# Kernel tuning notes

Hardware: AMD Instinct MI355X
Metric: run time of the kernel (lower is better)

## Reference

```python
import jax, jax.numpy as jnp
import numpy as np

DIM = 512
HEADS = 8
HD = DIM // HEADS
HIDDEN = 4 * DIM
EPS = 1e-5


def layernorm(x, g, b):
    mu = jnp.mean(x, axis=-1, keepdims=True)
    var = jnp.mean(jnp.square(x - mu), axis=-1, keepdims=True)
    return (x - mu) * jax.lax.rsqrt(var + EPS) * g + b


def setup_inputs() -> dict:
    key = jax.random.key(0)
    ks = jax.random.split(key, 10)
    B, P, N, C = 16, 4, 256, DIM
    s = 1.0 / np.sqrt(C)
    sh = 1.0 / np.sqrt(HIDDEN)
    return {
        "x": jax.random.normal(ks[0], (B, P, N, C), jnp.float32),
        "ln1_g": jnp.ones((C,), jnp.float32),
        "ln1_b": jnp.zeros((C,), jnp.float32),
        "w_qkv": jax.random.uniform(ks[1], (3 * C, C), jnp.float32, -s, s),
        "w_proj": jax.random.uniform(ks[2], (C, C), jnp.float32, -s, s),
        "b_proj": jax.random.uniform(ks[3], (C,), jnp.float32, -s, s),
        "ln2_g": jnp.ones((C,), jnp.float32),
        "ln2_b": jnp.zeros((C,), jnp.float32),
        "w1": jax.random.uniform(ks[4], (HIDDEN, C), jnp.float32, -s, s),
        "b1": jax.random.uniform(ks[5], (HIDDEN,), jnp.float32, -s, s),
        "w2": jax.random.uniform(ks[6], (C, HIDDEN), jnp.float32, -sh, sh),
        "b2": jax.random.uniform(ks[7], (C,), jnp.float32, -sh, sh),
    }


def reference(x, ln1_g, ln1_b, w_qkv, w_proj, b_proj, ln2_g, ln2_b, w1, b1, w2, b2):
    B, P, N, C = x.shape
    # --- attention branch (batched over B, P, heads; same math as the unrolled loops) ---
    h = layernorm(x, ln1_g, ln1_b)
    qkv = jnp.einsum('bpnc,dc->bpnd', h, w_qkv)            # [B,P,N,3C]
    qkv = qkv.reshape(B, P, N, 3, HEADS, HD)
    q, k, v = qkv[..., 0, :, :], qkv[..., 1, :, :], qkv[..., 2, :, :]  # [B,P,N,H,hd]
    scale = HD ** -0.5
    attn = jnp.einsum('bpnhd,bpmhd->bphnm', q * scale, k)  # [B,P,H,N,N]
    attn = jax.nn.softmax(attn, axis=-1)
    o = jnp.einsum('bphnm,bpmhd->bpnhd', attn, v).reshape(B, P, N, C)
    o = jnp.einsum('bpnc,dc->bpnd', o, w_proj) + b_proj
    x = x + o
    # --- MLP branch ---
    h = layernorm(x, ln2_g, ln2_b)
    h = jax.nn.gelu(jnp.einsum('bpnc,hc->bpnh', h, w1) + b1, approximate=False)
    h = jnp.einsum('bpnh,ch->bpnc', h, w2) + b2
    return x + h
```

## Files before the change

kernel.cpp:

```cpp
#include <hip/hip_runtime.h>

typedef __attribute__((ext_vector_type(8))) short short8;
typedef __attribute__((ext_vector_type(4))) float f32x4;
typedef __attribute__((ext_vector_type(4))) unsigned short u16x4;
typedef __attribute__((ext_vector_type(2))) unsigned int u32x2;
typedef __attribute__((ext_vector_type(4))) unsigned int u32x4;

__device__ __forceinline__ float bf2f(unsigned short u) {
    return __uint_as_float(((unsigned)u) << 16);
}
__device__ __forceinline__ unsigned short f2bf(float f) {
    unsigned u = __float_as_uint(f);
    u += 0x7fffu + ((u >> 16) & 1u);
    return (unsigned short)(u >> 16);
}
__device__ __forceinline__ unsigned pack2(float a, float b) {
    unsigned r;
    asm("v_cvt_pk_bf16_f32 %0, %1, %2" : "=v"(r) : "v"(a), "v"(b));
    return r;
}
__device__ __forceinline__ void load_lds16(const void* g, void* l) {
    __builtin_amdgcn_global_load_lds(
        (const __attribute__((address_space(1))) void*)g,
        (__attribute__((address_space(3))) void*)l, 16, 0, 0);
}
__device__ __forceinline__ bool is_bf16(const unsigned* dt) {
    return *dt == 0x3F803F80u;
}
__device__ __forceinline__ float gelu_fast(float t) {
    float q = t * (1.5957691f + 0.07135482f * t * t);
    float e = __expf(-q);
    return __fdividef(t, 1.0f + e);
}

__global__ __launch_bounds__(512) void cast_all(
    const void* s_wqkv, const void* s_wproj, const void* s_w1, const void* s_w2,
    const void* v0, const void* v1, const void* v2, const void* v3,
    const void* v4, const void* v5, const void* v6,
    unsigned short* d_wqkv, unsigned short* d_wproj, unsigned short* d_w1,
    unsigned short* d_w2, unsigned short* par, const unsigned* dt)
{
    bool isbf = is_bf16(dt);
    int b = blockIdx.x, tid = threadIdx.x;
    if (b < 768) {
        const void* src; unsigned short* dst; int off;
        if (b < 192)      { src = s_wqkv;  dst = d_wqkv;  off = b * 4096; }
        else if (b < 256) { src = s_wproj; dst = d_wproj; off = (b - 192) * 4096; }
        else if (b < 512) { src = s_w1;    dst = d_w1;    off = (b - 256) * 4096; }
        else              { src = s_w2;    dst = d_w2;    off = (b - 512) * 4096; }
        int i = off + tid * 8;
        if (isbf) {
            *(short8*)(dst + i) = *(const short8*)((const unsigned short*)src + i);
        } else {
            const float* s = (const float*)src + i;
            short8 o;
            #pragma unroll
            for (int j = 0; j < 8; ++j) o[j] = (short)f2bf(s[j]);
            *(short8*)(dst + i) = o;
        }
    } else {
        const void* srcs[7]  = {v0, v1, v2, v3, v4, v5, v6};
        const int   sizes[7] = {512, 512, 512, 512, 512, 2048, 512};
        const int   offs[7]  = {0, 512, 1024, 1536, 2048, 2560, 4608};
        int j = b - 768;
        const void* s = srcs[j];
        unsigned short* d = par + offs[j];
        for (int i = tid; i < sizes[j]; i += 512)
            d[i] = isbf ? ((const unsigned short*)s)[i] : f2bf(((const float*)s)[i]);
    }
}

__global__ __launch_bounds__(256) void ln_kernel(
    const void* __restrict__ xin, size_t row0, int isf32,
    const unsigned short* __restrict__ g, const unsigned short* __restrict__ b,
    unsigned short* __restrict__ y)
{
    int w = threadIdx.x >> 6, lane = threadIdx.x & 63;
    size_t lr = (size_t)blockIdx.x * 4 + w;
    size_t gr = row0 + lr;
    float v[8];
    if (isf32) {
        const float* xr = (const float*)xin + (gr << 9) + (lane << 3);
        #pragma unroll
        for (int j = 0; j < 8; ++j) v[j] = xr[j];
    } else {
        short8 raw = *(const short8*)((const unsigned short*)xin + (gr << 9) + (lane << 3));
        #pragma unroll
        for (int j = 0; j < 8; ++j) v[j] = bf2f((unsigned short)raw[j]);
    }
    float sum = 0.f, sq = 0.f;
    #pragma unroll
    for (int j = 0; j < 8; ++j) { sum += v[j]; sq += v[j] * v[j]; }
    #pragma unroll
    for (int off = 32; off > 0; off >>= 1) {
        sum += __shfl_xor(sum, off);
        sq  += __shfl_xor(sq, off);
    }
    float mu  = sum * (1.0f / 512.0f);
    float var = sq * (1.0f / 512.0f) - mu * mu;
    float rs  = rsqrtf(var + 1e-5f);
    short8 gr8 = *(const short8*)(g + (lane << 3));
    short8 br8 = *(const short8*)(b + (lane << 3));
    float o[8];
    #pragma unroll
    for (int j = 0; j < 8; ++j)
        o[j] = (v[j] - mu) * rs * bf2f((unsigned short)gr8[j]) + bf2f((unsigned short)br8[j]);
    u32x4 ov = {pack2(o[0], o[1]), pack2(o[2], o[3]),
                pack2(o[4], o[5]), pack2(o[6], o[7])};
    *(u32x4*)(y + (lr << 9) + (lane << 3)) = ov;
}

__global__ __launch_bounds__(256, 2) void gemm_big(
    const unsigned short* __restrict__ A, const unsigned short* __restrict__ W,
    const unsigned short* __restrict__ bias,
    unsigned short* __restrict__ out,
    int NBY, int N, int K, int mode)
{
    __shared__ char lds[49152];

    int tid = threadIdx.x;
    int w = tid >> 6, lane = tid & 63;
    int l15 = lane & 15, g = lane >> 4;

    int L = blockIdx.x;
    int bx, by;
    if ((NBY & 7) == 0) {
        int nby8 = NBY >> 3;
        int xcd = L & 7, i = L >> 3;
        by = xcd * nby8 + (i % nby8);
        bx = i / nby8;
    } else {
        by = L % NBY;
        bx = L / NBY;
    }
    int m0 = by << 8, n0 = bx << 7;
    int wm = (w >> 1) << 7;
    int wn = (w & 1) << 6;

    int srow = tid >> 3;
    int u = (tid & 7) ^ (srow & 7);
    const unsigned short* gA[8];
    const unsigned short* gB[4];
    #pragma unroll
    for (int j = 0; j < 8; ++j)
        gA[j] = A + (size_t)(m0 + j * 32 + srow) * K + u * 8;
    #pragma unroll
    for (int j = 0; j < 4; ++j)
        gB[j] = W + (size_t)(n0 + j * 32 + srow) * K + u * 8;
    int lslot = tid * 16;
    int swz = l15 & 7;

    f32x4 acc[4][8];
    #pragma unroll
    for (int i = 0; i < 4; ++i)
        #pragma unroll
        for (int j = 0; j < 8; ++j) acc[i][j] = (f32x4){0.f, 0.f, 0.f, 0.f};

    for (int k = 0; k < K; k += 64) {
        if (k > 0) __syncthreads();
        #pragma unroll
        for (int j = 0; j < 8; ++j)
            load_lds16(gA[j] + k, &lds[j * 4096 + lslot]);
        #pragma unroll
        for (int j = 0; j < 4; ++j)
            load_lds16(gB[j] + k, &lds[32768 + j * 4096 + lslot]);
        __syncthreads();
        const char* bAct = lds;
        const char* bW = lds + 32768;
        #pragma unroll
        for (int s = 0; s < 2; ++s) {
            int cs = ((s * 4 + g) ^ swz) << 4;
            short8 wf[4];
            #pragma unroll
            for (int i = 0; i < 4; ++i)
                wf[i] = *(const short8*)(bW + (wn + i * 16 + l15) * 128 + cs);
            #pragma unroll
            for (int jg = 0; jg < 8; jg += 4) {
                short8 af[4];
                #pragma unroll
                for (int j = 0; j < 4; ++j)
                    af[j] = *(const short8*)(bAct + (wm + (jg + j) * 16 + l15) * 128 + cs);
                #pragma unroll
                for (int i = 0; i < 4; ++i)
                    #pragma unroll
                    for (int j = 0; j < 4; ++j)
                        acc[i][jg + j] = __builtin_amdgcn_mfma_f32_16x16x32_bf16(
                            wf[i], af[j], acc[i][jg + j], 0, 0, 0);
            }
        }
    }
    __syncthreads();

    if (mode == 2) {
        #pragma unroll
        for (int i = 0; i < 4; ++i) {
            u16x4 bb = *(const u16x4*)(bias + n0 + wn + i * 16 + g * 4);
            #pragma unroll
            for (int j = 0; j < 8; ++j)
                #pragma unroll
                for (int r = 0; r < 4; ++r)
                    acc[i][j][r] = gelu_fast(acc[i][j][r] + bf2f(bb[r]));
        }
    }

    #pragma unroll
    for (int hh = 0; hh < 2; ++hh) {
        if ((w >> 1) == hh) {
            #pragma unroll
            for (int j = 0; j < 8; ++j) {
                int mloc = j * 16 + l15;
                char* rowp = lds + mloc * 256;
                int sw = mloc & 30;
                #pragma unroll
                for (int i = 0; i < 4; ++i) {
                    int cq = (wn + i * 16 + g * 4) >> 2;
                    u32x2 pk = {pack2(acc[i][j][0], acc[i][j][1]),
                                pack2(acc[i][j][2], acc[i][j][3])};
                    *(u32x2*)(rowp + ((cq ^ sw) << 3)) = pk;
                }
            }
        }
        __syncthreads();
        int rL = tid >> 4, lc = tid & 15;
        int colg = n0 + lc * 8;
        #pragma unroll
        for (int ps = 0; ps < 8; ++ps) {
            int row = ps * 16 + rL;
            int rowL = m0 + hh * 128 + row;
            int c16 = lc ^ ((row >> 1) & 15);
            short8 vv = *(const short8*)(lds + row * 256 + (c16 << 4));
            *(short8*)(out + (size_t)rowL * N + colg) = vv;
        }
        if (hh == 0) __syncthreads();
    }
}

__global__ __launch_bounds__(256) void gemm8(
    const unsigned short* __restrict__ A, const unsigned short* __restrict__ W,
    const unsigned short* __restrict__ bias,
    const void* __restrict__ resid, size_t rrow0,
    void* __restrict__ out, size_t orow0,
    int NBY, int N, int K, int mode, int inbf)
{
    constexpr int BN = 128;
    __shared__ char lds[32768];

    int tid = threadIdx.x;
    int w = tid >> 6, lane = tid & 63;
    int l15 = lane & 15, g = lane >> 4;

    int L = blockIdx.x;
    int bx, by;
    if ((NBY & 7) == 0) {
        int nby8 = NBY >> 3;
        int xcd = L & 7, i = L >> 3;
        by = xcd * nby8 + (i % nby8);
        bx = i / nby8;
    } else {
        by = L % NBY;
        bx = L / NBY;
    }
    int m0 = by << 7, n0 = bx << 7;
    int wm = (w >> 1) << 6;
    int wn = (w & 1) << 6;

    int srow_t = tid >> 3;
    int u_t = (tid & 7) ^ (srow_t & 7);
    const unsigned short* gA[4];
    const unsigned short* gB[4];
    #pragma unroll
    for (int j = 0; j < 4; ++j) {
        gA[j] = A + (size_t)(m0 + j * 32 + srow_t) * K + u_t * 8;
        gB[j] = W + (size_t)(n0 + j * 32 + srow_t) * K + u_t * 8;
    }
    int lslot = tid * 16;
    int swz = l15 & 7;

    f32x4 acc[4][4];
    #pragma unroll
    for (int i = 0; i < 4; ++i)
        #pragma unroll
        for (int j = 0; j < 4; ++j) acc[i][j] = (f32x4){0.f, 0.f, 0.f, 0.f};

    for (int k = 0; k < K; k += 64) {
        if (k > 0) __syncthreads();
        #pragma unroll
        for (int j = 0; j < 4; ++j) {
            load_lds16(gA[j] + k, &lds[j * 4096 + lslot]);
            load_lds16(gB[j] + k, &lds[16384 + j * 4096 + lslot]);
        }
        __syncthreads();
        const char* bAct = lds;
        const char* bW = bAct + 16384;
        #pragma unroll
        for (int s = 0; s < 2; ++s) {
            int cs = ((s * 4 + g) ^ swz) << 4;
            short8 wf[4], af[4];
            #pragma unroll
            for (int i = 0; i < 4; ++i)
                wf[i] = *(const short8*)(bW + (wn + i * 16 + l15) * 128 + cs);
            #pragma unroll
            for (int j = 0; j < 4; ++j)
                af[j] = *(const short8*)(bAct + (wm + j * 16 + l15) * 128 + cs);
            #pragma unroll
            for (int i = 0; i < 4; ++i)
                #pragma unroll
                for (int j = 0; j < 4; ++j)
                    acc[i][j] = __builtin_amdgcn_mfma_f32_16x16x32_bf16(wf[i], af[j], acc[i][j], 0, 0, 0);
        }
    }
    __syncthreads();

    char* tb = (char*)lds;
    #pragma unroll
    for (int j = 0; j < 4; ++j) {
        int mloc = wm + j * 16 + l15;
        char* rowp = tb + mloc * (BN * 2);
        int sw = mloc & (BN / 4 - 2);
        #pragma unroll
        for (int i = 0; i < 4; ++i) {
            int cq = (wn + i * 16 + g * 4) >> 2;
            u32x2 pk = {pack2(acc[i][j][0], acc[i][j][1]),
                        pack2(acc[i][j][2], acc[i][j][3])};
            *(u32x2*)(rowp + ((cq ^ sw) << 3)) = pk;
        }
    }
    __syncthreads();

    int rL = tid >> 4;
    int lc = tid & 15;
    int colg = n0 + lc * 8;
    float bv[8];
    if (mode != 0) {
        short8 bb = *(const short8*)(bias + colg);
        #pragma unroll
        for (int t = 0; t < 8; ++t) bv[t] = bf2f((unsigned short)bb[t]);
    }

    #pragma unroll
    for (int ps = 0; ps < 8; ++ps) {
        int row = ps * 16 + rL;
        int rowL = m0 + row;
        int c16 = lc ^ ((row >> 1) & 15);
        short8 vv = *(const short8*)(tb + row * (BN * 2) + (c16 << 4));

        if (mode == 0) {
            *(short8*)((unsigned short*)out + (size_t)rowL * N + colg) = vv;
        } else if (mode == 1) {
            size_t rbase = (rrow0 + rowL) * (size_t)N + colg;
            float o8[8];
            if (inbf) {
                short8 rr = *(const short8*)((const unsigned short*)resid + rbase);
                #pragma unroll
                for (int t = 0; t < 8; ++t)
                    o8[t] = bf2f((unsigned short)rr[t]) + bf2f((unsigned short)vv[t]) + bv[t];
            } else {
                f32x4 r0 = *(const f32x4*)((const float*)resid + rbase);
                f32x4 r1 = *(const f32x4*)((const float*)resid + rbase + 4);
                #pragma unroll
                for (int t = 0; t < 4; ++t) {
                    o8[t]     = r0[t] + bf2f((unsigned short)vv[t]) + bv[t];
                    o8[t + 4] = r1[t] + bf2f((unsigned short)vv[t + 4]) + bv[t + 4];
                }
            }
            u32x4 ov = {pack2(o8[0], o8[1]), pack2(o8[2], o8[3]),
                        pack2(o8[4], o8[5]), pack2(o8[6], o8[7])};
            *(u32x4*)((unsigned short*)out + (size_t)rowL * N + colg) = ov;
        } else {
            size_t rbase = (size_t)rowL * N + colg;
            short8 rr = *(const short8*)((const unsigned short*)resid + rbase);
            float o8[8];
            #pragma unroll
            for (int t = 0; t < 8; ++t)
                o8[t] = bf2f((unsigned short)rr[t]) + bf2f((unsigned short)vv[t]) + bv[t];
            size_t obase = (orow0 + rowL) * (size_t)N + colg;
            if (inbf) {
                u32x4 ov = {pack2(o8[0], o8[1]), pack2(o8[2], o8[3]),
                            pack2(o8[4], o8[5]), pack2(o8[6], o8[7])};
                *(u32x4*)((unsigned short*)out + obase) = ov;
            } else {
                float* ob = (float*)out + obase;
                *(f32x4*)ob       = (f32x4){o8[0], o8[1], o8[2], o8[3]};
                *(f32x4*)(ob + 4) = (f32x4){o8[4], o8[5], o8[6], o8[7]};
            }
        }
    }
}

__global__ __launch_bounds__(256) void attn_mfma(
    const unsigned short* __restrict__ qkv, unsigned short* __restrict__ o)
{
    __shared__ unsigned short Vt[64 * 256];
    __shared__ unsigned short Ps[4][16 * 256];
    int bp = blockIdx.x >> 3, h = blockIdx.x & 7;
    const unsigned short* base = qkv + (size_t)bp * 256 * 1536;
    int qo = h << 6, ko = 512 + (h << 6), vo = 1024 + (h << 6);
    int tid = threadIdx.x, w = tid >> 6, lane = tid & 63;
    int l15 = lane & 15, g = lane >> 4;

    {
        int d0 = (tid & 7) * 8;
        int sb = tid >> 3;
        #pragma unroll
        for (int r = 0; r < 8; ++r) {
            int s = sb + r * 32;
            short8 v = *(const short8*)(base + (size_t)s * 1536 + vo + d0);
            char* pbase = (char*)Vt + ((s & 7) << 1);
            int srow = s >> 3;
            #pragma unroll
            for (int j = 0; j < 8; ++j)
                *(unsigned short*)(pbase + (d0 + j) * 512 + ((srow ^ j) << 4)) =
                    (unsigned short)v[j];
        }
    }
    __syncthreads();

    short8 kb[16][2];
    #pragma unroll
    for (int ns = 0; ns < 16; ++ns)
        #pragma unroll
        for (int t = 0; t < 2; ++t)
            kb[ns][t] = *(const short8*)(base + (size_t)(ns * 16 + l15) * 1536 + ko + t * 32 + g * 8);

    unsigned short* P = Ps[w];

    for (int pass = 0; pass < 4; ++pass) {
        int q0 = pass * 64 + w * 16;
        short8 qa[2];
        #pragma unroll
        for (int t = 0; t < 2; ++t)
            qa[t] = *(const short8*)(base + (size_t)(q0 + l15) * 1536 + qo + t * 32 + g * 8);
        f32x4 S[16];
        #pragma unroll
        for (int ns = 0; ns < 16; ++ns) {
            f32x4 a = {0.f, 0.f, 0.f, 0.f};
            #pragma unroll
            for (int t = 0; t < 2; ++t)
                a = __builtin_amdgcn_mfma_f32_16x16x32_bf16(qa[t], kb[ns][t], a, 0, 0, 0);
            S[ns] = a;
        }
        float mx[4], sums[4], inv[4];
        #pragma unroll
        for (int r = 0; r < 4; ++r) {
            float m = -1e30f;
            #pragma unroll
            for (int ns = 0; ns < 16; ++ns) m = fmaxf(m, S[ns][r]);
            m *= 0.125f;
            #pragma unroll
            for (int off = 1; off < 16; off <<= 1) m = fmaxf(m, __shfl_xor(m, off));
            mx[r] = m;
            sums[r] = 0.f;
        }
        #pragma unroll
        for (int ns = 0; ns < 16; ++ns)
            #pragma unroll
            for (int r = 0; r < 4; ++r) {
                float p = __expf(S[ns][r] * 0.125f - mx[r]);
                sums[r] += p;
                S[ns][r] = p;
            }
        #pragma unroll
        for (int r = 0; r < 4; ++r) {
            float s2 = sums[r];
            #pragma unroll
            for (int off = 1; off < 16; off <<= 1) s2 += __shfl_xor(s2, off);
            inv[r] = 1.0f / s2;
        }
        #pragma unroll
        for (int ns = 0; ns < 16; ++ns)
            #pragma unroll
            for (int r = 0; r < 4; ++r) {
                int mq = g * 4 + r;
                int s = ns * 16 + l15;
                *(unsigned short*)((char*)P + mq * 512 + (((s >> 3) ^ (mq & 7)) << 4) + ((s & 7) << 1))
                    = f2bf(S[ns][r] * inv[r]);
            }
        f32x4 O[4];
        #pragma unroll
        for (int ds = 0; ds < 4; ++ds) O[ds] = (f32x4){0.f, 0.f, 0.f, 0.f};
        #pragma unroll
        for (int ks = 0; ks < 8; ++ks) {
            int c = (ks * 4 + g) ^ (l15 & 7);
            short8 pa = *(const short8*)((const char*)P + l15 * 512 + (c << 4));
            #pragma unroll
            for (int ds = 0; ds < 4; ++ds) {
                short8 vb = *(const short8*)((const char*)Vt + (ds * 16 + l15) * 512 + (c << 4));
                O[ds] = __builtin_amdgcn_mfma_f32_16x16x32_bf16(pa, vb, O[ds], 0, 0, 0);
            }
        }
        #pragma unroll
        for (int ds = 0; ds < 4; ++ds)
            #pragma unroll
            for (int r = 0; r < 4; ++r) {
                int mq = q0 + g * 4 + r;
                int d = ds * 16 + l15;
                o[((size_t)(bp * 256 + mq) << 9) + (h << 6) + d] = f2bf(O[ds][r]);
            }
    }
}

extern "C" void kernel_launch(void* const* d_in, const int* in_sizes, int n_in,
                              void* d_out, int out_size, void* d_ws, size_t ws_size,
                              hipStream_t stream)
{
    const void* x      = d_in[0];
    const void* ln1_g  = d_in[1];
    const void* ln1_b  = d_in[2];
    const void* w_qkv  = d_in[3];
    const void* w_proj = d_in[4];
    const void* b_proj = d_in[5];
    const void* ln2_g  = d_in[6];
    const void* ln2_b  = d_in[7];
    const void* w1     = d_in[8];
    const void* b1     = d_in[9];
    const void* w2     = d_in[10];
    const void* b2     = d_in[11];
    const unsigned* dt = (const unsigned*)ln1_g;

    const int isbf = (in_sizes[1] == 512 * 2);

    const int M = 16384;
    char* ws = (char*)d_ws;
    unsigned short* wqkv_b  = (unsigned short*)(ws);
    unsigned short* wproj_b = (unsigned short*)(ws + 1572864);
    unsigned short* w1_b    = (unsigned short*)(ws + 2097152);
    unsigned short* w2_b    = (unsigned short*)(ws + 4194304);
    unsigned short* par     = (unsigned short*)(ws + 6291456);
    const size_t CAST_END = 6308096;

    const unsigned short* p_wqkv  = isbf ? (const unsigned short*)w_qkv  : wqkv_b;
    const unsigned short* p_wproj = isbf ? (const unsigned short*)w_proj : wproj_b;
    const unsigned short* p_w1    = isbf ? (const unsigned short*)w1     : w1_b;
    const unsigned short* p_w2    = isbf ? (const unsigned short*)w2     : w2_b;
    const unsigned short* p_g1    = isbf ? (const unsigned short*)ln1_g  : par + 0;
    const unsigned short* p_b1ln  = isbf ? (const unsigned short*)ln1_b  : par + 512;
    const unsigned short* p_bproj = isbf ? (const unsigned short*)b_proj : par + 1024;
    const unsigned short* p_g2    = isbf ? (const unsigned short*)ln2_g  : par + 1536;
    const unsigned short* p_b2ln  = isbf ? (const unsigned short*)ln2_b  : par + 2048;
    const unsigned short* p_b1    = isbf ? (const unsigned short*)b1     : par + 2560;
    const unsigned short* p_b2    = isbf ? (const unsigned short*)b2     : par + 4608;

    int NC = 64;
    const int cand[7] = {1, 2, 4, 8, 16, 32, 64};
    for (int i = 0; i < 7; ++i) {
        size_t need = CAST_END + (size_t)(M / cand[i]) * 10240;
        if (need <= ws_size) { NC = cand[i]; break; }
    }
    const int R = M / NC;

    char* cb = ws + CAST_END;
    unsigned short* h   = (unsigned short*)(cb);
    unsigned short* qkv = (unsigned short*)(cb + (size_t)R * 1024);
    unsigned short* o   = (unsigned short*)(cb + (size_t)R * 4096);
    unsigned short* x2  = (unsigned short*)(cb + (size_t)R * 5120);
    unsigned short* hid = (unsigned short*)(cb + (size_t)R * 6144);
    unsigned short* h2  = h;

    if (!isbf) {
        cast_all<<<775, 512, 0, stream>>>(w_qkv, w_proj, w1, w2,
                                          ln1_g, ln1_b, b_proj, ln2_g, ln2_b, b1, b2,
                                          wqkv_b, wproj_b, w1_b, w2_b, par, dt);
    }

    for (int c = 0; c < NC; ++c) {
        const size_t r0 = (size_t)c * R;
        const int NBY  = R / 128;
        const int NBY2 = R / 256;

        ln_kernel<<<R / 4, 256, 0, stream>>>(x, r0, isbf ? 0 : 1, p_g1, p_b1ln, h);
        gemm8<<<(1536 / 128) * NBY, 256, 0, stream>>>(
            h, p_wqkv, nullptr, nullptr, 0, qkv, 0, NBY, 1536, 512, 0, isbf);
        attn_mfma<<<(R / 256) * 8, 256, 0, stream>>>(qkv, o);
        gemm8<<<(512 / 128) * NBY, 256, 0, stream>>>(
            o, p_wproj, p_bproj, x, r0, x2, 0, NBY, 512, 512, 1, isbf);
        ln_kernel<<<R / 4, 256, 0, stream>>>(x2, 0, 0, p_g2, p_b2ln, h2);
        gemm_big<<<(2048 / 128) * NBY2, 256, 0, stream>>>(
            h2, p_w1, p_b1, hid, NBY2, 2048, 512, 2);
        gemm8<<<(512 / 128) * NBY, 256, 0, stream>>>(
            hid, p_w2, p_b2, x2, 0, d_out, r0, NBY, 512, 2048, 3, isbf);
    }
}
```

Measured before the change: 307.4 us.

## Rewrite MLP up-projection GEMM as 256x256 tile with double-buffered LDS pipeline

```diff
diff --git a/kernel.cpp b/kernel.cpp
--- a/kernel.cpp
+++ b/kernel.cpp
@@ -110,13 +110,13 @@
     *(u32x4*)(y + (lr << 9) + (lane << 3)) = ov;
 }
 
-__global__ __launch_bounds__(256, 2) void gemm_big(
+__global__ __launch_bounds__(512, 2) void gemm_256(
     const unsigned short* __restrict__ A, const unsigned short* __restrict__ W,
     const unsigned short* __restrict__ bias,
     unsigned short* __restrict__ out,
     int NBY, int N, int K, int mode)
 {
-    __shared__ char lds[49152];
+    __shared__ char lds[131072];
 
     int tid = threadIdx.x;
     int w = tid >> 6, lane = tid & 63;
@@ -133,20 +133,19 @@
         by = L % NBY;
         bx = L / NBY;
     }
-    int m0 = by << 8, n0 = bx << 7;
-    int wm = (w >> 1) << 7;
-    int wn = (w & 1) << 6;
+    int m0 = by << 8, n0 = bx << 8;
+    int wm = (w >> 2) << 7;
+    int wn = (w & 3) << 6;
 
     int srow = tid >> 3;
     int u = (tid & 7) ^ (srow & 7);
-    const unsigned short* gA[8];
+    const unsigned short* gA[4];
     const unsigned short* gB[4];
     #pragma unroll
-    for (int j = 0; j < 8; ++j)
-        gA[j] = A + (size_t)(m0 + j * 32 + srow) * K + u * 8;
-    #pragma unroll
-    for (int j = 0; j < 4; ++j)
-        gB[j] = W + (size_t)(n0 + j * 32 + srow) * K + u * 8;
+    for (int j = 0; j < 4; ++j) {
+        gA[j] = A + (size_t)(m0 + j * 64 + srow) * K + u * 8;
+        gB[j] = W + (size_t)(n0 + j * 64 + srow) * K + u * 8;
+    }
     int lslot = tid * 16;
     int swz = l15 & 7;
 
@@ -156,40 +155,78 @@
         #pragma unroll
         for (int j = 0; j < 8; ++j) acc[i][j] = (f32x4){0.f, 0.f, 0.f, 0.f};
 
-    for (int k = 0; k < K; k += 64) {
-        if (k > 0) __syncthreads();
-        #pragma unroll
-        for (int j = 0; j < 8; ++j)
-            load_lds16(gA[j] + k, &lds[j * 4096 + lslot]);
-        #pragma unroll
-        for (int j = 0; j < 4; ++j)
-            load_lds16(gB[j] + k, &lds[32768 + j * 4096 + lslot]);
-        __syncthreads();
-        const char* bAct = lds;
-        const char* bW = lds + 32768;
-        #pragma unroll
-        for (int s = 0; s < 2; ++s) {
-            int cs = ((s * 4 + g) ^ swz) << 4;
-            short8 wf[4];
-            #pragma unroll
-            for (int i = 0; i < 4; ++i)
-                wf[i] = *(const short8*)(bW + (wn + i * 16 + l15) * 128 + cs);
-            #pragma unroll
-            for (int jg = 0; jg < 8; jg += 4) {
-                short8 af[4];
-                #pragma unroll
-                for (int j = 0; j < 4; ++j)
-                    af[j] = *(const short8*)(bAct + (wm + (jg + j) * 16 + l15) * 128 + cs);
-                #pragma unroll
-                for (int i = 0; i < 4; ++i)
+    #pragma unroll
+    for (int j = 0; j < 4; ++j) {
+        load_lds16(gA[j], &lds[j * 8192 + lslot]);
+        load_lds16(gB[j], &lds[32768 + j * 8192 + lslot]);
+    }
+    asm volatile("s_waitcnt vmcnt(0)" ::: "memory");
+    __builtin_amdgcn_s_barrier();
+    __builtin_amdgcn_sched_barrier(0);
+
+    int nk = K >> 6;
+    int p = 0;
+    for (int T = 0; T < nk; ++T) {
+        const char* bA = &lds[p * 65536];
+        const char* bW = bA + 32768;
+        char* nb = &lds[(p ^ 1) * 65536];
+        bool hn = (T + 1 < nk);
+        int kn = (T + 1) << 6;
+
+        short8 bf[4][2];
+        #pragma unroll
+        for (int q = 0; q < 4; ++q) {
+            if (q == 0) {
+                #pragma unroll
+                for (int s = 0; s < 2; ++s) {
+                    int cs = ((s * 4 + g) ^ swz) << 4;
                     #pragma unroll
-                    for (int j = 0; j < 4; ++j)
-                        acc[i][jg + j] = __builtin_amdgcn_mfma_f32_16x16x32_bf16(
-                            wf[i], af[j], acc[i][jg + j], 0, 0, 0);
-            }
-        }
-    }
-    __syncthreads();
+                    for (int i = 0; i < 4; ++i)
+                        bf[i][s] = *(const short8*)(bW + (wn + i * 16 + l15) * 128 + cs);
+                }
+            }
+            short8 af[2][2];
+            #pragma unroll
+            for (int s = 0; s < 2; ++s) {
+                int cs = ((s * 4 + g) ^ swz) << 4;
+                #pragma unroll
+                for (int jj = 0; jj < 2; ++jj)
+                    af[jj][s] = *(const short8*)(bA + (wm + (2 * q + jj) * 16 + l15) * 128 + cs);
+            }
+            if (hn) {
+                if (q == 0) {
+                    load_lds16(gA[0] + kn, nb + lslot);
+                    load_lds16(gA[1] + kn, nb + 8192 + lslot);
+                    load_lds16(gA[2] + kn, nb + 16384 + lslot);
+                } else if (q == 1) {
+                    load_lds16(gA[3] + kn, nb + 24576 + lslot);
+                    load_lds16(gB[0] + kn, nb + 32768 + lslot);
+                    load_lds16(gB[1] + kn, nb + 40960 + lslot);
+                } else if (q == 2) {
+                    load_lds16(gB[2] + kn, nb + 49152 + lslot);
+                    load_lds16(gB[3] + kn, nb + 57344 + lslot);
+                }
+            }
+            __builtin_amdgcn_s_barrier();
+            asm volatile("s_waitcnt lgkmcnt(0)" ::: "memory");
+            __builtin_amdgcn_sched_barrier(0);
+            __builtin_amdgcn_s_setprio(1);
+            #pragma unroll
+            for (int s = 0; s < 2; ++s)
+                #pragma unroll
+                for (int jj = 0; jj < 2; ++jj)
+                    #pragma unroll
+                    for (int i = 0; i < 4; ++i)
+                        acc[i][2 * q + jj] = __builtin_amdgcn_mfma_f32_16x16x32_bf16(
+                            bf[i][s], af[jj][s], acc[i][2 * q + jj], 0, 0, 0);
+            __builtin_amdgcn_s_setprio(0);
+            if (q == 3 && hn)
+                asm volatile("s_waitcnt vmcnt(0)" ::: "memory");
+            __builtin_amdgcn_s_barrier();
+            __builtin_amdgcn_sched_barrier(0);
+        }
+        p ^= 1;
+    }
 
     if (mode == 2) {
         #pragma unroll
@@ -205,12 +242,12 @@
 
     #pragma unroll
     for (int hh = 0; hh < 2; ++hh) {
-        if ((w >> 1) == hh) {
+        if ((w >> 2) == hh) {
             #pragma unroll
             for (int j = 0; j < 8; ++j) {
                 int mloc = j * 16 + l15;
-                char* rowp = lds + mloc * 256;
-                int sw = mloc & 30;
+                char* rowp = (char*)lds + mloc * 512;
+                int sw = mloc & 62;
                 #pragma unroll
                 for (int i = 0; i < 4; ++i) {
                     int cq = (wn + i * 16 + g * 4) >> 2;
@@ -221,14 +258,14 @@
             }
         }
         __syncthreads();
-        int rL = tid >> 4, lc = tid & 15;
+        int rL = tid >> 5, lc = tid & 31;
         int colg = n0 + lc * 8;
         #pragma unroll
         for (int ps = 0; ps < 8; ++ps) {
             int row = ps * 16 + rL;
             int rowL = m0 + hh * 128 + row;
-            int c16 = lc ^ ((row >> 1) & 15);
-            short8 vv = *(const short8*)(lds + row * 256 + (c16 << 4));
+            int c16 = lc ^ ((row >> 1) & 31);
+            short8 vv = *(const short8*)((char*)lds + row * 512 + (c16 << 4));
             *(short8*)(out + (size_t)rowL * N + colg) = vv;
         }
         if (hh == 0) __syncthreads();
@@ -574,7 +611,7 @@
         gemm8<<<(512 / 128) * NBY, 256, 0, stream>>>(
             o, p_wproj, p_bproj, x, r0, x2, 0, NBY, 512, 512, 1, isbf);
         ln_kernel<<<R / 4, 256, 0, stream>>>(x2, 0, 0, p_g2, p_b2ln, h2);
-        gemm_big<<<(2048 / 128) * NBY2, 256, 0, stream>>>(
+        gemm_256<<<(2048 / 256) * NBY2, 512, 0, stream>>>(
             h2, p_w1, p_b1, hid, NBY2, 2048, 512, 2);
         gemm8<<<(512 / 128) * NBY, 256, 0, stream>>>(
             hid, p_w2, p_b2, x2, 0, d_out, r0, NBY, 512, 2048, 3, isbf);
```

After: 315.9 us. 2.8% more time.
